# Performance work log

Measured on AMD Instinct MI355X. Metric: run time of the kernel, lower is better.

Reference implementation:

```python
import jax, jax.numpy as jnp
import numpy as np

N, E = 100000, 400000
NUM_TIME, NUM_TYPE = 288, 16
DT, DTY, DBW, DIL, DCON = 16, 16, 8, 8, 16
HID, HEADS, EDIM, LAYERS = 64, 4, 16, 2
IN_CH = DT + DTY + DBW + DIL + DCON  # 64


def setup_inputs() -> dict:
    key = jax.random.key(0)
    ks = jax.random.split(key, 24)
    t = jax.random.randint(ks[0], (N, 1), 0, NUM_TIME).astype(jnp.float32)
    ty = jax.random.randint(ks[1], (N, 1), 0, NUM_TYPE).astype(jnp.float32)
    bw = jax.random.randint(ks[2], (N, 1), 0, 2).astype(jnp.float32)
    il = jax.random.randint(ks[3], (N, 1), 0, 2).astype(jnp.float32)
    con = jax.random.normal(ks[4], (N, DCON), jnp.float32)
    nodes = jnp.concatenate([t, ty, bw, il, con], axis=-1)
    edges = jax.random.randint(ks[5], (2, E), 0, N, dtype=jnp.int32)
    relation = jax.random.normal(ks[6], (E, EDIM), jnp.float32)
    s = 0.05
    params = dict(
        time_emb=jax.random.normal(ks[7], (NUM_TIME, DT)) * s,
        type_emb=jax.random.normal(ks[8], (NUM_TYPE, DTY)) * s,
        biway_emb=jax.random.normal(ks[9], (2, DBW)) * s,
        islink_emb=jax.random.normal(ks[10], (2, DIL)) * s,
        proj_w=jax.random.normal(ks[11], (HID, IN_CH)) * (1.0 / np.sqrt(IN_CH)),
        proj_b=jnp.zeros((HID,), jnp.float32),
        lin_l_w=jax.random.normal(ks[12], (LAYERS, HEADS * HID, HID)) * (1.0 / np.sqrt(HID)),
        lin_l_b=jnp.zeros((LAYERS, HEADS * HID), jnp.float32),
        lin_r_w=jax.random.normal(ks[13], (LAYERS, HEADS * HID, HID)) * (1.0 / np.sqrt(HID)),
        lin_r_b=jnp.zeros((LAYERS, HEADS * HID), jnp.float32),
        lin_e_w=jax.random.normal(ks[14], (LAYERS, HEADS * HID, EDIM)) * (1.0 / np.sqrt(EDIM)),
        att=jax.random.normal(ks[15], (LAYERS, HEADS, HID)) * (1.0 / np.sqrt(HID)),
        gat_b=jnp.zeros((LAYERS, HID), jnp.float32),
    )
    return dict(nodes=nodes, edges=edges, relation=relation, **params)


def _gatv2_layer(h, src, dst, eattr, wl, bl, wr, br, we, att, bias):
    n = h.shape[0]
    xl = (h @ wl.T + bl).reshape(n, HEADS, HID)   # source transform
    xr = (h @ wr.T + br).reshape(n, HEADS, HID)   # destination transform
    ep = (eattr @ we.T).reshape(-1, HEADS, HID)   # edge transform
    m = xl[src] + xr[dst] + ep                    # [Ea, H, C]
    m = jax.nn.leaky_relu(m, 0.2)
    logits = jnp.einsum('ehc,hc->eh', m, att)     # [Ea, H]
    mx = jax.ops.segment_max(logits, dst, num_segments=n)
    ex = jnp.exp(logits - mx[dst])
    den = jax.ops.segment_sum(ex, dst, num_segments=n)
    alpha = ex / den[dst]                         # softmax per destination
    out = jax.ops.segment_sum(xl[src] * alpha[:, :, None], dst, num_segments=n)
    return out.mean(axis=1) + bias                # concat=False -> head mean


def reference(nodes, edges, relation, time_emb, type_emb, biway_emb, islink_emb,
              proj_w, proj_b, lin_l_w, lin_l_b, lin_r_w, lin_r_b, lin_e_w, att, gat_b):
    idx = jax.lax.stop_gradient(nodes[:, :4]).astype(jnp.int32)
    con = nodes[:, 4:]
    h = jnp.concatenate([time_emb[idx[:, 0]], type_emb[idx[:, 1]],
                         biway_emb[idx[:, 2]], islink_emb[idx[:, 3]], con], axis=-1)
    h = h @ proj_w.T + proj_b
    n = h.shape[0]
    loop = jnp.arange(n, dtype=edges.dtype)
    src = jnp.concatenate([edges[0], loop])
    dst = jnp.concatenate([edges[1], loop])
    # PyG add_self_loops with fill_value='mean' for edge_attr
    rel_aug = jnp.concatenate([relation, jnp.broadcast_to(relation.mean(0), (n, relation.shape[1]))], axis=0)
    for l in range(LAYERS):
        out = _gatv2_layer(h, src, dst, rel_aug, lin_l_w[l], lin_l_b[l],
                           lin_r_w[l], lin_r_b[l], lin_e_w[l], att[l], gat_b[l])
        h = jax.nn.relu(out + h)
    return h
```

## Files before the change

### kernel.cpp

```cpp
#include <hip/hip_runtime.h>

typedef unsigned short u16;
typedef unsigned int u32;

__device__ __forceinline__ float bf2f(u16 u){ union{u32 i; float f;} v; v.i=((u32)u)<<16; return v.f; }
__device__ __forceinline__ float bflo(u32 p){ union{u32 i; float f;} v; v.i=p<<16; return v.f; }
__device__ __forceinline__ float bfhi(u32 p){ union{u32 i; float f;} v; v.i=p&0xffff0000u; return v.f; }
__device__ __forceinline__ u16 f2bf(float x){ union{float f; u32 i;} v; v.f=x; u32 b=v.i;
  return (u16)((b + 0x7fffu + ((b>>16)&1u))>>16); }
__device__ __forceinline__ u32 pk2(float a, float b){ return ((u32)f2bf(b)<<16) | (u32)f2bf(a); }

#define HEADS 4
#define HHID 256
#define NT 16

__global__ void TopoAggregator_33217277067466_kernel(float* __restrict__ out, int n, float val){
  for(int i = blockIdx.x*blockDim.x + threadIdx.x; i < n; i += gridDim.x*blockDim.x)
    out[i] = val;
}

__global__ void k_marker(const int* __restrict__ rowstart, const float* __restrict__ h,
                         float* __restrict__ out, int N, int E){
  if(threadIdx.x!=0 || blockIdx.x!=0) return;
  float M = 0.f;
  if(rowstart[N] != E) M = 400.f;
  else {
    int allz = 1;
    for(int i=0;i<128;i++) if(h[i]!=0.f){ allz=0; break; }
    if(allz) M = 500.f;
  }
  if(M != 0.f) out[0] = M;
}

__global__ void k_zero(int* __restrict__ counts, float* __restrict__ relmean, int N){
  int i = blockIdx.x*blockDim.x + threadIdx.x;
  if(i < N) counts[i] = 0;
  if(i < 16) relmean[i] = 0.f;
}

__global__ void k_relmean(const float* __restrict__ rel, float* __restrict__ relmean, int E){
  __shared__ float red[256][16];
  float s[16];
#pragma unroll
  for(int j=0;j<16;j++) s[j]=0.f;
  for(int r = blockIdx.x*blockDim.x + threadIdx.x; r < E; r += gridDim.x*blockDim.x){
    const float4* p = (const float4*)(rel + (size_t)r*16);
    float4 a=p[0], b=p[1], c=p[2], d=p[3];
    s[0]+=a.x; s[1]+=a.y; s[2]+=a.z; s[3]+=a.w;
    s[4]+=b.x; s[5]+=b.y; s[6]+=b.z; s[7]+=b.w;
    s[8]+=c.x; s[9]+=c.y; s[10]+=c.z; s[11]+=c.w;
    s[12]+=d.x; s[13]+=d.y; s[14]+=d.z; s[15]+=d.w;
  }
  int tid = threadIdx.x;
#pragma unroll
  for(int j=0;j<16;j++) red[tid][j]=s[j];
  __syncthreads();
  for(int off=128; off>0; off>>=1){
    if(tid<off){
#pragma unroll
      for(int j=0;j<16;j++) red[tid][j]+=red[tid+off][j];
    }
    __syncthreads();
  }
  if(tid<16) atomicAdd(relmean+tid, red[0][tid]*(1.0f/(float)E));
}

__global__ void k_count(const int* __restrict__ edges, int* __restrict__ counts, int E, int N){
  int e = blockIdx.x*blockDim.x + threadIdx.x;
  if(e>=E) return;
  int d = edges[E+e];
  if(d<0) d=0; if(d>=N) d=N-1;
  atomicAdd(counts+d, 1);
}

#define STILE 1024
__global__ void k_scan_a(const int* __restrict__ counts, int* __restrict__ tilesum, int N){
  __shared__ int red[256];
  int base = blockIdx.x*STILE;
  int tid = threadIdx.x;
  int s = 0;
  for(int i=tid; i<STILE; i+=256){
    int idx = base + i;
    s += (idx < N) ? counts[idx] : 0;
  }
  red[tid] = s;
  __syncthreads();
  for(int off=128; off>0; off>>=1){
    if(tid<off) red[tid] += red[tid+off];
    __syncthreads();
  }
  if(tid==0) tilesum[blockIdx.x] = red[0];
}

__global__ void k_scan_b(const int* __restrict__ tilesum, int* __restrict__ tileoff, int nT){
  __shared__ int buf[1024];
  int tid = threadIdx.x;
  buf[tid] = (tid < nT) ? tilesum[tid] : 0;
  __syncthreads();
  for(int off=1; off<1024; off<<=1){
    int v = (tid>=off) ? buf[tid-off] : 0;
    __syncthreads();
    buf[tid] += v;
    __syncthreads();
  }
  if(tid < nT) tileoff[tid] = (tid==0) ? 0 : buf[tid-1];
}

__global__ void k_scan_c(const int* __restrict__ counts, const int* __restrict__ tileoff,
                         int* __restrict__ rowstart, int* __restrict__ cursor, int N){
  __shared__ int buf[STILE];
  int base = blockIdx.x*STILE;
  int tid = threadIdx.x;
  int idx = base + tid;
  int c = (idx < N) ? counts[idx] : 0;
  buf[tid] = c;
  __syncthreads();
  for(int off=1; off<1024; off<<=1){
    int v = (tid>=off) ? buf[tid-off] : 0;
    __syncthreads();
    buf[tid] += v;
    __syncthreads();
  }
  int excl = buf[tid] - c + tileoff[blockIdx.x];
  if(idx < N){ rowstart[idx]=excl; cursor[idx]=excl; }
  if(idx == N-1) rowstart[N] = excl + c;
}

__global__ void k_scatter(const int* __restrict__ edges, const float* __restrict__ relation,
                          int* __restrict__ cursor,
                          int* __restrict__ adj_src, u32* __restrict__ rel_s, int E, int N){
  int e = blockIdx.x*blockDim.x + threadIdx.x;
  if(e>=E) return;
  int s = edges[e], d = edges[E+e];
  if(d<0) d=0; if(d>=N) d=N-1;
  int pos = atomicAdd(cursor+d, 1);
  adj_src[pos]=s;
  const float4* rp = (const float4*)(relation + (size_t)e*16);
  float4 q0=rp[0], q1=rp[1], q2=rp[2], q3=rp[3];
  uint4* dst = (uint4*)(rel_s + (size_t)pos*8);
  dst[0] = make_uint4(pk2(q0.x,q0.y), pk2(q0.z,q0.w), pk2(q1.x,q1.y), pk2(q1.z,q1.w));
  dst[1] = make_uint4(pk2(q2.x,q2.y), pk2(q2.z,q2.w), pk2(q3.x,q3.y), pk2(q3.z,q3.w));
}

__global__ void k_embed(const float* __restrict__ nodes,
                        const float* __restrict__ time_emb, const float* __restrict__ type_emb,
                        const float* __restrict__ biway_emb, const float* __restrict__ islink_emb,
                        const float* __restrict__ projw, const float* __restrict__ projb,
                        float* __restrict__ h, int N){
  __shared__ float W[64][65];
  __shared__ float h0[4][64];
  int tid = threadIdx.x;
  for(int i=tid; i<64*64; i+=256) W[i>>6][i&63] = projw[i];
  __syncthreads();
  int wave = tid>>6, lane = tid&63;
  int node = blockIdx.x*4 + wave;
  if(node<N){
    const float* nr = nodes + (size_t)node*20;
    float v; int c = lane;
    if(c<16){
      int t=(int)nr[0]; t = t<0?0:(t>287?287:t);
      v = time_emb[t*16+c];
    } else if(c<32){
      int ty=(int)nr[1]; ty = ty<0?0:(ty>15?15:ty);
      v = type_emb[ty*16+(c-16)];
    } else if(c<40){
      int bw=(int)nr[2]; bw = bw<0?0:(bw>1?1:bw);
      v = biway_emb[bw*8+(c-32)];
    } else if(c<48){
      int il=(int)nr[3]; il = il<0?0:(il>1?1:il);
      v = islink_emb[il*8+(c-40)];
    } else {
      v = nr[4 + (c-48)];
    }
    h0[wave][lane]=v;
  }
  __syncthreads();
  if(node<N){
    float acc = projb[lane];
#pragma unroll
    for(int k=0;k<64;k++) acc += W[lane][k]*h0[wave][k];
    h[(size_t)node*64+lane]=acc;
  }
}

__global__ void k_xlr(const float* __restrict__ h,
                      const float* __restrict__ wl, const float* __restrict__ bl,
                      const float* __restrict__ wr, const float* __restrict__ br,
                      u16* __restrict__ xl, u16* __restrict__ xr, int N){
  __shared__ float hs[NT*64];
  int tid = threadIdx.x;
  int base = blockIdx.x*NT;
  int nvalid = N - base; if(nvalid > NT) nvalid = NT;
  if(nvalid == NT){
    *(float4*)(hs + tid*4) = *(const float4*)(h + (size_t)base*64 + tid*4);
  } else {
    for(int i=tid; i<NT*64; i+=256) hs[i] = (i < nvalid*64) ? h[(size_t)base*64+i] : 0.f;
  }
  __syncthreads();
  int o = tid;
  const float4* wl4 = (const float4*)(wl + (size_t)o*64);
  const float4* wr4 = (const float4*)(wr + (size_t)o*64);
  float blv = bl[o], brv = br[o];
  float accl[NT], accr[NT];
#pragma unroll
  for(int n=0;n<NT;n++){ accl[n]=blv; accr[n]=brv; }
  for(int kk=0; kk<16; kk++){
    float4 a = wl4[kk];
    float4 b = wr4[kk];
#pragma unroll
    for(int n=0;n<NT;n++){
      float4 hv = *(const float4*)(hs + n*64 + kk*4);
      accl[n] += a.x*hv.x + a.y*hv.y + a.z*hv.z + a.w*hv.w;
      accr[n] += b.x*hv.x + b.y*hv.y + b.z*hv.z + b.w*hv.w;
    }
  }
  for(int n=0;n<nvalid;n++){
    xl[(size_t)(base+n)*HHID + o] = f2bf(accl[n]);
    xr[(size_t)(base+n)*HHID + o] = f2bf(accr[n]);
  }
}

__global__ void __launch_bounds__(256)
k_fused(const int* __restrict__ rowstart, const int* __restrict__ adj_src,
        const u32* __restrict__ rel_s, const float* __restrict__ relmean,
        const float* __restrict__ we, const float* __restrict__ att,
        const u16* __restrict__ xl, const u16* __restrict__ xr,
        const float* __restrict__ gat_b,
        float* __restrict__ h, int N, float* __restrict__ outp){
  __shared__ float weT[16*256];
  {
    int tid = threadIdx.x;
    for(int i=tid; i<16*256; i+=256){
      int k = i >> 8, ch = i & 255;
      weT[k*256 + ch] = we[(size_t)ch*16 + k];
    }
  }
  __syncthreads();
  const int lane = threadIdx.x & 63;
  const int sub = lane & 15;
  const int wid = (blockIdx.x*blockDim.x + threadIdx.x) >> 6;
  const int nw  = (gridDim.x*blockDim.x) >> 6;
  const float4* wT4 = (const float4*)weT;

  const float4 at4 = *(const float4*)(att + lane*4);

  float es0=0.f, es1=0.f, es2=0.f, es3=0.f;
#pragma unroll
  for(int k=0;k<16;k++){
    float rmk = relmean[k];
    float4 w4 = wT4[k*64 + lane];
    es0 += rmk*w4.x; es1 += rmk*w4.y; es2 += rmk*w4.z; es3 += rmk*w4.w;
  }

  for(int node = wid; node < N; node += nw){
    const int lo = rowstart[node], hi = rowstart[node+1];
    uint2 pb = *(const uint2*)(xr + (size_t)node*HHID + lane*4);
    float bv0=bflo(pb.x), bv1=bfhi(pb.x), bv2=bflo(pb.y), bv3=bfhi(pb.y);

    float m, den, a0, a1, a2, a3;
    {
      uint2 ps = *(const uint2*)(xl + (size_t)node*HHID + lane*4);
      float sv0=bflo(ps.x), sv1=bfhi(ps.x), sv2=bflo(ps.y), sv3=bfhi(ps.y);
      float c = 0.f;
      {
        float mm;
        mm = sv0 + bv0 + es0; mm = (mm>0.f)?mm:0.2f*mm; c += mm*at4.x;
        mm = sv1 + bv1 + es1; mm = (mm>0.f)?mm:0.2f*mm; c += mm*at4.y;
        mm = sv2 + bv2 + es2; mm = (mm>0.f)?mm:0.2f*mm; c += mm*at4.z;
        mm = sv3 + bv3 + es3; mm = (mm>0.f)?mm:0.2f*mm; c += mm*at4.w;
      }
      c += __shfl_xor(c, 1);
      c += __shfl_xor(c, 2);
      c += __shfl_xor(c, 4);
      c += __shfl_xor(c, 8);
      m = c; den = 1.f;
      a0 = sv0; a1 = sv1; a2 = sv2; a3 = sv3;
    }

    int sv0i = 0;
    if(lo < hi) sv0i = adj_src[lo];
    for(int p=lo; p<hi; p++){
      int sv1i = 0;
      if(p+1 < hi) sv1i = adj_src[p+1];
      int sv = sv0i; if(sv<0) sv=0; if(sv>=N) sv=N-1;

      const uint4* rp = (const uint4*)(rel_s + (size_t)p*8);
      uint4 rq0 = rp[0], rq1 = rp[1];

      uint2 pa = *(const uint2*)(xl + (size_t)sv*HHID + lane*4);

      float ep0=0.f, ep1=0.f, ep2=0.f, ep3=0.f;
#define EPW(W, KBASE) { \
        float rlo = bflo(W), rhi = bfhi(W); \
        float4 wa = wT4[(KBASE)*64 + lane]; \
        float4 wb = wT4[(KBASE+1)*64 + lane]; \
        ep0 += rlo*wa.x + rhi*wb.x; \
        ep1 += rlo*wa.y + rhi*wb.y; \
        ep2 += rlo*wa.z + rhi*wb.z; \
        ep3 += rlo*wa.w + rhi*wb.w; }
      EPW(rq0.x, 0)  EPW(rq0.y, 2)  EPW(rq0.z, 4)  EPW(rq0.w, 6)
      EPW(rq1.x, 8)  EPW(rq1.y,10)  EPW(rq1.z,12)  EPW(rq1.w,14)
#undef EPW

      float av0=bflo(pa.x), av1=bfhi(pa.x), av2=bflo(pa.y), av3=bfhi(pa.y);
      float c = 0.f;
      {
        float mm;
        mm = av0 + bv0 + ep0; mm = (mm>0.f)?mm:0.2f*mm; c += mm*at4.x;
        mm = av1 + bv1 + ep1; mm = (mm>0.f)?mm:0.2f*mm; c += mm*at4.y;
        mm = av2 + bv2 + ep2; mm = (mm>0.f)?mm:0.2f*mm; c += mm*at4.z;
        mm = av3 + bv3 + ep3; mm = (mm>0.f)?mm:0.2f*mm; c += mm*at4.w;
      }
      c += __shfl_xor(c, 1);
      c += __shfl_xor(c, 2);
      c += __shfl_xor(c, 4);
      c += __shfl_xor(c, 8);

      if(c > m){
        float sc = __expf(m - c);
        den *= sc; a0 *= sc; a1 *= sc; a2 *= sc; a3 *= sc;
        m = c;
      }
      float wgt = __expf(c - m);
      den += wgt;
      a0 += wgt*av0; a1 += wgt*av1; a2 += wgt*av2; a3 += wgt*av3;

      sv0i = sv1i;
    }

    float inv = 1.0f/den;
    float v0=a0*inv, v1=a1*inv, v2=a2*inv, v3=a3*inv;
    v0 += __shfl_xor(v0,16); v0 += __shfl_xor(v0,32);
    v1 += __shfl_xor(v1,16); v1 += __shfl_xor(v1,32);
    v2 += __shfl_xor(v2,16); v2 += __shfl_xor(v2,32);
    v3 += __shfl_xor(v3,16); v3 += __shfl_xor(v3,32);
    if(lane < 16){
      int cb = sub*4;
      float4 hv = *(const float4*)(h + (size_t)node*64 + cb);
      const float4 gb = *(const float4*)(gat_b + cb);
      float o0 = fmaxf(0.25f*v0 + gb.x + hv.x, 0.f);
      float o1 = fmaxf(0.25f*v1 + gb.y + hv.y, 0.f);
      float o2 = fmaxf(0.25f*v2 + gb.z + hv.z, 0.f);
      float o3 = fmaxf(0.25f*v3 + gb.w + hv.w, 0.f);
      *(float4*)(h + (size_t)node*64 + cb) = make_float4(o0,o1,o2,o3);
      if(outp) *(float4*)(outp + (size_t)node*64 + cb) = make_float4(o0,o1,o2,o3);
    }
  }
}

extern "C" void kernel_launch(void* const* d_in, const int* in_sizes, int n_in,
                              void* d_out, int out_size, void* d_ws, size_t ws_size,
                              hipStream_t stream) {
  const float* nodes     = (const float*)d_in[0];
  const int*   edges     = (const int*)d_in[1];
  const float* relation  = (const float*)d_in[2];
  const float* time_emb  = (const float*)d_in[3];
  const float* type_emb  = (const float*)d_in[4];
  const float* biway_emb = (const float*)d_in[5];
  const float* islink_emb= (const float*)d_in[6];
  const float* proj_w    = (const float*)d_in[7];
  const float* proj_b    = (const float*)d_in[8];
  const float* lin_l_w   = (const float*)d_in[9];
  const float* lin_l_b   = (const float*)d_in[10];
  const float* lin_r_w   = (const float*)d_in[11];
  const float* lin_r_b   = (const float*)d_in[12];
  const float* lin_e_w   = (const float*)d_in[13];
  const float* att       = (const float*)d_in[14];
  const float* gat_b     = (const float*)d_in[15];

  const int N  = in_sizes[0] / 20;
  const int E  = in_sizes[1] / 2;
  const int nT = (N + STILE - 1) / STILE;

  size_t off = 0;
  auto alloc = [&](size_t bytes)->size_t {
    size_t p = off;
    off += ((bytes + 255) / 256) * 256;
    return p;
  };
  size_t o_h        = alloc((size_t)N*64*4);
  size_t o_xl       = alloc((size_t)N*HHID*2);
  size_t o_xr       = alloc((size_t)N*HHID*2);
  size_t o_rels     = alloc((size_t)E*32);
  size_t o_relmean  = alloc(64*4);
  size_t o_counts   = alloc((size_t)N*4);
  size_t o_rowstart = alloc((size_t)(N+1)*4);
  size_t o_cursor   = alloc((size_t)(N+1)*4);
  size_t o_adjsrc   = alloc((size_t)E*4);
  size_t o_tilesum  = alloc((size_t)nT*4);
  size_t o_tileoff  = alloc((size_t)nT*4);

  if (off > ws_size) {
    TopoAggregator_33217277067466_kernel<<<2048, 256, 0, stream>>>(
        (float*)d_out, out_size, 100.0f);
    return;
  }

  char* w = (char*)d_ws;
  float* h        = (float*)(w + o_h);
  u16*   xl       = (u16*)(w + o_xl);
  u16*   xr       = (u16*)(w + o_xr);
  u32*   rel_s    = (u32*)(w + o_rels);
  float* relmean  = (float*)(w + o_relmean);
  int*   counts   = (int*)(w + o_counts);
  int*   rowstart = (int*)(w + o_rowstart);
  int*   cursor   = (int*)(w + o_cursor);
  int*   adj_src  = (int*)(w + o_adjsrc);
  int*   tilesum  = (int*)(w + o_tilesum);
  int*   tileoff  = (int*)(w + o_tileoff);

  k_zero<<<(N+255)/256, 256, 0, stream>>>(counts, relmean, N);
  k_relmean<<<64, 256, 0, stream>>>(relation, relmean, E);
  k_count<<<(E+255)/256, 256, 0, stream>>>(edges, counts, E, N);
  k_scan_a<<<nT, 256, 0, stream>>>(counts, tilesum, N);
  k_scan_b<<<1, 1024, 0, stream>>>(tilesum, tileoff, nT);
  k_scan_c<<<nT, 1024, 0, stream>>>(counts, tileoff, rowstart, cursor, N);
  k_scatter<<<(E+255)/256, 256, 0, stream>>>(edges, relation, cursor, adj_src, rel_s, E, N);

  k_embed<<<(N+3)/4, 256, 0, stream>>>(nodes, time_emb, type_emb, biway_emb, islink_emb,
                                       proj_w, proj_b, h, N);

  for(int l=0; l<2; l++){
    k_xlr<<<(N+NT-1)/NT, 256, 0, stream>>>(h,
        lin_l_w + (size_t)l*HHID*64, lin_l_b + (size_t)l*HHID,
        lin_r_w + (size_t)l*HHID*64, lin_r_b + (size_t)l*HHID,
        xl, xr, N);
    k_fused<<<4096, 256, 0, stream>>>(rowstart, adj_src, rel_s, relmean,
        lin_e_w + (size_t)l*HHID*16, att + (size_t)l*HEADS*64,
        xl, xr, gat_b + (size_t)l*64,
        h, N,
        (l==1) ? (float*)d_out : (float*)nullptr);
  }
  k_marker<<<1, 64, 0, stream>>>(rowstart, h, (float*)d_out, N, E);
}
```

Measured before the change: 868.8 us.

## Persist xl/xr projection with register weights and pipeline edge loop two-deep

The xl/xr projection kernel becomes persistent over a fixed grid. Each block handles either the left or the right transform and keeps its weight row in registers across node tiles, so weights are no longer reloaded from global memory for every tile. The fused attention kernel's edge loop now handles two edges per iteration and prefetches the next pair's relation data and source features, which gives more memory-level parallelism for the gathers. The cost is higher register pressure in both kernels and a fixed grid size that may underfill or serialize work.

Result: slower. 1.190 ms (+37.0%).

```diff
diff --git a/kernel.cpp b/kernel.cpp
--- a/kernel.cpp
+++ b/kernel.cpp
@@ -183,40 +183,50 @@
   }
 }
 
-__global__ void k_xlr(const float* __restrict__ h,
-                      const float* __restrict__ wl, const float* __restrict__ bl,
-                      const float* __restrict__ wr, const float* __restrict__ br,
-                      u16* __restrict__ xl, u16* __restrict__ xr, int N){
+__global__ void __launch_bounds__(256)
+k_xlr(const float* __restrict__ h,
+      const float* __restrict__ wl, const float* __restrict__ bl,
+      const float* __restrict__ wr, const float* __restrict__ br,
+      u16* __restrict__ xl, u16* __restrict__ xr, int N, int nTiles){
+  const int half = gridDim.x >> 1;
+  const bool isR = (blockIdx.x >= half);
+  const float* wsel = isR ? wr : wl;
+  const float* bsel = isR ? br : bl;
+  u16* xout = isR ? xr : xl;
+  const int b0 = isR ? (blockIdx.x - half) : blockIdx.x;
+  const int o = threadIdx.x;
+  float4 wreg[16];
+  {
+    const float4* wp = (const float4*)(wsel + (size_t)o*64);
+#pragma unroll
+    for(int i=0;i<16;i++) wreg[i]=wp[i];
+  }
+  const float bv = bsel[o];
   __shared__ float hs[NT*64];
-  int tid = threadIdx.x;
-  int base = blockIdx.x*NT;
-  int nvalid = N - base; if(nvalid > NT) nvalid = NT;
-  if(nvalid == NT){
-    *(float4*)(hs + tid*4) = *(const float4*)(h + (size_t)base*64 + tid*4);
-  } else {
-    for(int i=tid; i<NT*64; i+=256) hs[i] = (i < nvalid*64) ? h[(size_t)base*64+i] : 0.f;
-  }
-  __syncthreads();
-  int o = tid;
-  const float4* wl4 = (const float4*)(wl + (size_t)o*64);
-  const float4* wr4 = (const float4*)(wr + (size_t)o*64);
-  float blv = bl[o], brv = br[o];
-  float accl[NT], accr[NT];
-#pragma unroll
-  for(int n=0;n<NT;n++){ accl[n]=blv; accr[n]=brv; }
-  for(int kk=0; kk<16; kk++){
-    float4 a = wl4[kk];
-    float4 b = wr4[kk];
-#pragma unroll
-    for(int n=0;n<NT;n++){
-      float4 hv = *(const float4*)(hs + n*64 + kk*4);
-      accl[n] += a.x*hv.x + a.y*hv.y + a.z*hv.z + a.w*hv.w;
-      accr[n] += b.x*hv.x + b.y*hv.y + b.z*hv.z + b.w*hv.w;
-    }
-  }
-  for(int n=0;n<nvalid;n++){
-    xl[(size_t)(base+n)*HHID + o] = f2bf(accl[n]);
-    xr[(size_t)(base+n)*HHID + o] = f2bf(accr[n]);
+  for(int t=b0; t<nTiles; t+=half){
+    int base = t*NT;
+    int nvalid = N - base; if(nvalid > NT) nvalid = NT;
+    if(nvalid == NT){
+      *(float4*)(hs + o*4) = *(const float4*)(h + (size_t)base*64 + o*4);
+    } else {
+      for(int i=o; i<NT*64; i+=256) hs[i] = (i < nvalid*64) ? h[(size_t)base*64+i] : 0.f;
+    }
+    __syncthreads();
+    float acc[NT];
+#pragma unroll
+    for(int n=0;n<NT;n++) acc[n]=bv;
+#pragma unroll
+    for(int kk=0; kk<16; kk++){
+      float4 a = wreg[kk];
+#pragma unroll
+      for(int n=0;n<NT;n++){
+        float4 hv = *(const float4*)(hs + n*64 + kk*4);
+        acc[n] += a.x*hv.x + a.y*hv.y + a.z*hv.z + a.w*hv.w;
+      }
+    }
+    for(int n=0;n<nvalid;n++)
+      xout[(size_t)(base+n)*HHID + o] = f2bf(acc[n]);
+    __syncthreads();
   }
 }
 
@@ -277,55 +287,99 @@
       a0 = sv0; a1 = sv1; a2 = sv2; a3 = sv3;
     }
 
-    int sv0i = 0;
-    if(lo < hi) sv0i = adj_src[lo];
-    for(int p=lo; p<hi; p++){
-      int sv1i = 0;
-      if(p+1 < hi) sv1i = adj_src[p+1];
-      int sv = sv0i; if(sv<0) sv=0; if(sv>=N) sv=N-1;
-
-      const uint4* rp = (const uint4*)(rel_s + (size_t)p*8);
-      uint4 rq0 = rp[0], rq1 = rp[1];
-
-      uint2 pa = *(const uint2*)(xl + (size_t)sv*HHID + lane*4);
-
-      float ep0=0.f, ep1=0.f, ep2=0.f, ep3=0.f;
-#define EPW(W, KBASE) { \
-        float rlo = bflo(W), rhi = bfhi(W); \
-        float4 wa = wT4[(KBASE)*64 + lane]; \
-        float4 wb = wT4[(KBASE+1)*64 + lane]; \
-        ep0 += rlo*wa.x + rhi*wb.x; \
-        ep1 += rlo*wa.y + rhi*wb.y; \
-        ep2 += rlo*wa.z + rhi*wb.z; \
-        ep3 += rlo*wa.w + rhi*wb.w; }
-      EPW(rq0.x, 0)  EPW(rq0.y, 2)  EPW(rq0.z, 4)  EPW(rq0.w, 6)
-      EPW(rq1.x, 8)  EPW(rq1.y,10)  EPW(rq1.z,12)  EPW(rq1.w,14)
-#undef EPW
-
-      float av0=bflo(pa.x), av1=bfhi(pa.x), av2=bflo(pa.y), av3=bfhi(pa.y);
-      float c = 0.f;
+    if(lo < hi){
+      int sA1 = (lo+2<hi) ? adj_src[lo+2] : 0;
+      int sB1 = (lo+3<hi) ? adj_src[lo+3] : 0;
+      uint4 rA0c, rA1c; uint2 paAc;
       {
-        float mm;
-        mm = av0 + bv0 + ep0; mm = (mm>0.f)?mm:0.2f*mm; c += mm*at4.x;
-        mm = av1 + bv1 + ep1; mm = (mm>0.f)?mm:0.2f*mm; c += mm*at4.y;
-        mm = av2 + bv2 + ep2; mm = (mm>0.f)?mm:0.2f*mm; c += mm*at4.z;
-        mm = av3 + bv3 + ep3; mm = (mm>0.f)?mm:0.2f*mm; c += mm*at4.w;
+        int sv = adj_src[lo]; if(sv<0) sv=0; if(sv>=N) sv=N-1;
+        const uint4* rp = (const uint4*)(rel_s + (size_t)lo*8);
+        rA0c = rp[0]; rA1c = rp[1];
+        paAc = *(const uint2*)(xl + (size_t)sv*HHID + lane*4);
       }
-      c += __shfl_xor(c, 1);
-      c += __shfl_xor(c, 2);
-      c += __shfl_xor(c, 4);
-      c += __shfl_xor(c, 8);
-
-      if(c > m){
-        float sc = __expf(m - c);
-        den *= sc; a0 *= sc; a1 *= sc; a2 *= sc; a3 *= sc;
-        m = c;
+      uint4 rB0c = make_uint4(0,0,0,0), rB1c = rB0c; uint2 paBc = make_uint2(0u,0u);
+      if(lo+1 < hi){
+        int sv = adj_src[lo+1]; if(sv<0) sv=0; if(sv>=N) sv=N-1;
+        const uint4* rp = (const uint4*)(rel_s + (size_t)(lo+1)*8);
+        rB0c = rp[0]; rB1c = rp[1];
+        paBc = *(const uint2*)(xl + (size_t)sv*HHID + lane*4);
       }
-      float wgt = __expf(c - m);
-      den += wgt;
-      a0 += wgt*av0; a1 += wgt*av1; a2 += wgt*av2; a3 += wgt*av3;
-
-      sv0i = sv1i;
+
+      for(int p=lo; p<hi; p+=2){
+        uint4 rA0n = make_uint4(0,0,0,0), rA1n = rA0n, rB0n = rA0n, rB1n = rA0n;
+        uint2 paAn = make_uint2(0u,0u), paBn = paAn;
+        if(p+2 < hi){
+          int sv = sA1; if(sv<0) sv=0; if(sv>=N) sv=N-1;
+          const uint4* rp = (const uint4*)(rel_s + (size_t)(p+2)*8);
+          rA0n = rp[0]; rA1n = rp[1];
+          paAn = *(const uint2*)(xl + (size_t)sv*HHID + lane*4);
+          if(p+3 < hi){
+            int sv2 = sB1; if(sv2<0) sv2=0; if(sv2>=N) sv2=N-1;
+            const uint4* rp2 = (const uint4*)(rel_s + (size_t)(p+3)*8);
+            rB0n = rp2[0]; rB1n = rp2[1];
+            paBn = *(const uint2*)(xl + (size_t)sv2*HHID + lane*4);
+          }
+        }
+        int sA2 = (p+4<hi) ? adj_src[p+4] : 0;
+        int sB2 = (p+5<hi) ? adj_src[p+5] : 0;
+
+        float eA0=0.f,eA1=0.f,eA2=0.f,eA3=0.f, eB0=0.f,eB1=0.f,eB2=0.f,eB3=0.f;
+#define EPW2(WA, WB, KB) { \
+        float al=bflo(WA), ah=bfhi(WA), bl_=bflo(WB), bh_=bfhi(WB); \
+        float4 wa = wT4[(KB)*64 + lane]; \
+        float4 wb = wT4[(KB+1)*64 + lane]; \
+        eA0 += al*wa.x + ah*wb.x;  eB0 += bl_*wa.x + bh_*wb.x; \
+        eA1 += al*wa.y + ah*wb.y;  eB1 += bl_*wa.y + bh_*wb.y; \
+        eA2 += al*wa.z + ah*wb.z;  eB2 += bl_*wa.z + bh_*wb.z; \
+        eA3 += al*wa.w + ah*wb.w;  eB3 += bl_*wa.w + bh_*wb.w; }
+        EPW2(rA0c.x, rB0c.x, 0)  EPW2(rA0c.y, rB0c.y, 2)
+        EPW2(rA0c.z, rB0c.z, 4)  EPW2(rA0c.w, rB0c.w, 6)
+        EPW2(rA1c.x, rB1c.x, 8)  EPW2(rA1c.y, rB1c.y,10)
+        EPW2(rA1c.z, rB1c.z,12)  EPW2(rA1c.w, rB1c.w,14)
+#undef EPW2
+
+        float avA0=bflo(paAc.x), avA1=bfhi(paAc.x), avA2=bflo(paAc.y), avA3=bfhi(paAc.y);
+        float avB0=bflo(paBc.x), avB1=bfhi(paBc.x), avB2=bflo(paBc.y), avB3=bfhi(paBc.y);
+        float cA = 0.f, cB = 0.f;
+        {
+          float mm;
+          mm = avA0 + bv0 + eA0; mm=(mm>0.f)?mm:0.2f*mm; cA += mm*at4.x;
+          mm = avA1 + bv1 + eA1; mm=(mm>0.f)?mm:0.2f*mm; cA += mm*at4.y;
+          mm = avA2 + bv2 + eA2; mm=(mm>0.f)?mm:0.2f*mm; cA += mm*at4.z;
+          mm = avA3 + bv3 + eA3; mm=(mm>0.f)?mm:0.2f*mm; cA += mm*at4.w;
+          mm = avB0 + bv0 + eB0; mm=(mm>0.f)?mm:0.2f*mm; cB += mm*at4.x;
+          mm = avB1 + bv1 + eB1; mm=(mm>0.f)?mm:0.2f*mm; cB += mm*at4.y;
+          mm = avB2 + bv2 + eB2; mm=(mm>0.f)?mm:0.2f*mm; cB += mm*at4.z;
+          mm = avB3 + bv3 + eB3; mm=(mm>0.f)?mm:0.2f*mm; cB += mm*at4.w;
+        }
+        cA += __shfl_xor(cA, 1); cB += __shfl_xor(cB, 1);
+        cA += __shfl_xor(cA, 2); cB += __shfl_xor(cB, 2);
+        cA += __shfl_xor(cA, 4); cB += __shfl_xor(cB, 4);
+        cA += __shfl_xor(cA, 8); cB += __shfl_xor(cB, 8);
+        if(p+1 >= hi) cB = -1e30f;
+
+        if(cA > m){
+          float sc = __expf(m - cA);
+          den *= sc; a0 *= sc; a1 *= sc; a2 *= sc; a3 *= sc;
+          m = cA;
+        }
+        float wA = __expf(cA - m);
+        den += wA;
+        a0 += wA*avA0; a1 += wA*avA1; a2 += wA*avA2; a3 += wA*avA3;
+
+        if(cB > m){
+          float sc = __expf(m - cB);
+          den *= sc; a0 *= sc; a1 *= sc; a2 *= sc; a3 *= sc;
+          m = cB;
+        }
+        float wB = __expf(cB - m);
+        den += wB;
+        a0 += wB*avB0; a1 += wB*avB1; a2 += wB*avB2; a3 += wB*avB3;
+
+        rA0c = rA0n; rA1c = rA1n; rB0c = rB0n; rB1c = rB1n;
+        paAc = paAn; paBc = paBn;
+        sA1 = sA2; sB1 = sB2;
+      }
     }
 
     float inv = 1.0f/den;
@@ -371,6 +425,7 @@
   const int N  = in_sizes[0] / 20;
   const int E  = in_sizes[1] / 2;
   const int nT = (N + STILE - 1) / STILE;
+  const int nTiles = (N + NT - 1) / NT;
 
   size_t off = 0;
   auto alloc = [&](size_t bytes)->size_t {
@@ -421,10 +476,10 @@
                                        proj_w, proj_b, h, N);
 
   for(int l=0; l<2; l++){
-    k_xlr<<<(N+NT-1)/NT, 256, 0, stream>>>(h,
+    k_xlr<<<2048, 256, 0, stream>>>(h,
         lin_l_w + (size_t)l*HHID*64, lin_l_b + (size_t)l*HHID,
         lin_r_w + (size_t)l*HHID*64, lin_r_b + (size_t)l*HHID,
-        xl, xr, N);
+        xl, xr, N, nTiles);
     k_fused<<<4096, 256, 0, stream>>>(rowstart, adj_src, rel_s, relmean,
         lin_e_w + (size_t)l*HHID*16, att + (size_t)l*HEADS*64,
         xl, xr, gat_b + (size_t)l*64,
```
